# Optimization experiments

Measured on AMD Instinct MI355X. Metric: run time of the kernel, lower is better.

Reference implementation:

```python
import jax, jax.numpy as jnp
import numpy as np

EPSILON = 0.5
B, N0, N1, N_DIM = 128, 128, 128, 32


def setup_inputs() -> dict:
    key = jax.random.key(0)
    ks = jax.random.split(key, 7)
    X = jax.random.normal(ks[0], (B, N_DIM), dtype=jnp.float32)
    t = jax.random.uniform(ks[1], (1,), dtype=jnp.float32, minval=0.05, maxval=0.95)
    Mu0 = jax.random.normal(ks[2], (N0, N_DIM), dtype=jnp.float32)
    Mu1 = jax.random.normal(ks[3], (N1, N_DIM), dtype=jnp.float32)
    # positive diagonal variances
    S0 = jax.random.uniform(ks[4], (N0, N_DIM), dtype=jnp.float32) + 0.5
    S1 = jax.random.uniform(ks[5], (N1, N_DIM), dtype=jnp.float32) + 0.5
    # nonnegative coupling that sums to 1 (stand-in for the EMD plan)
    Lam = jax.random.uniform(ks[6], (N0, N1), dtype=jnp.float32)
    Lam = Lam / jnp.sum(Lam)
    return {"X": X, "t": t, "Mu0": Mu0, "Mu1": Mu1, "S0": S0, "S1": S1, "Lam": Lam}


def reference(X, t, Mu0, Mu1, S0, S1, Lam):
    """GMMflow.calc_u: Gaussian-mixture weighted drift u(X, t)."""
    eps = EPSILON
    t = t.reshape(())  # scalar time
    S0b = S0[:, None, :]   # [N0, 1, n]
    S1b = S1[None, :, :]   # [1, N1, n]
    Ds = jnp.sqrt(4.0 * S0b * S1b + eps ** 4)          # [N0, N1, n]
    Cs = 0.5 * (Ds - eps ** 2)
    Sigma = ((1 - t) ** 2) * S0b + (t ** 2) * S1b + 2 * t * (1 - t) * Cs + (eps ** 2) * t * (1 - t)
    Pt = t * S1b + (1 - t) * Cs
    Qt = (1 - t) * S0b + t * Cs
    St = Pt - Qt - (eps ** 2) * t
    Mut = (1 - t) * Mu0[:, None, :] + t * Mu1[None, :, :]   # [N0, N1, n]
    v = Mu1[None, :, :] - Mu0[:, None, :]                   # [N0, N1, n]
    K = St / Sigma                                          # [N0, N1, n]

    D = X[:, None, None, :] - Mut[None]                     # [B, N0, N1, n]
    U = K[None] * D + v[None]                               # [B, N0, N1, n]
    # Independent-Normal log_prob with the +n/2*log(2*pi) offset cancelled
    logw = jnp.sum(-0.5 * D * D / Sigma[None] - 0.5 * jnp.log(Sigma)[None], axis=-1)  # [B, N0, N1]
    W = jnp.exp(jnp.clip(logw, -50.0, 50.0)) * Lam[None]    # [B, N0, N1]

    num = jnp.einsum('bijn,bij->bn', U, W)                  # weighted drift sum
    den = jnp.sum(W, axis=(1, 2))                           # [B]
    return num / den[:, None]
```

## Files before the change

### kernel.cpp

```cpp
#include <hip/hip_runtime.h>
#include <math.h>

#define BB 128
#define ND 32
#define NIJ 16384
#define EPS2 0.25f
#define EPS4 0.0625f

#define TIJ 64
#define NBLK (NIJ / TIJ)
#define NTHR 512
#define ROWF 132

#define XS_OFF  8448
#define CC_OFF  13056
#define LAM_OFF 13120
#define LDS_FL  13184
#define STG_ROW 36

#define PART_STRIDE 4224
#define DEN_OFF_P 4096

__global__ __launch_bounds__(NTHR, 2) void gmm_fused(
    const float* __restrict__ Xg,
    const float* __restrict__ tptr,
    const float* __restrict__ Mu0, const float* __restrict__ Mu1,
    const float* __restrict__ S0,  const float* __restrict__ S1,
    const float* __restrict__ Lam,
    float* __restrict__ part)
{
    __shared__ __align__(16) float lds[LDS_FL];

    const int tid  = threadIdx.x;
    const int blk  = blockIdx.x;
    const int ij0g = blk * TIJ;
    const float t   = tptr[0];
    const float omt = 1.0f - t;

#pragma unroll
    for (int k = 0; k < (BB * ND) / NTHR; ++k) {
        const int idx = tid + k * NTHR;
        lds[XS_OFF + (idx >> 5) * STG_ROW + (idx & 31)] = Xg[idx];
    }

#pragma unroll
    for (int k = 0; k < (TIJ * ND) / NTHR; ++k) {
        const int idx = tid + k * NTHR;
        const int ijl = idx >> 5;
        const int n   = idx & 31;
        const int ij  = ij0g + ijl;
        const int i   = ij >> 7;
        const int j   = ij & 127;
        const float s0  = S0[i * ND + n];
        const float s1  = S1[j * ND + n];
        const float mu0 = Mu0[i * ND + n];
        const float mu1 = Mu1[j * ND + n];
        const float Ds  = sqrtf(4.0f * s0 * s1 + EPS4);
        const float Cs  = 0.5f * (Ds - EPS2);
        const float Sigma = omt * omt * s0 + t * t * s1
                          + 2.0f * t * omt * Cs + EPS2 * t * omt;
        const float St  = (t * s1 + omt * Cs) - (omt * s0 + t * Cs) - EPS2 * t;
        const float Mut = omt * mu0 + t * mu1;
        const float v   = mu1 - mu0;
        const float invS = 1.0f / Sigma;
        const float Kf  = St * invS;
        const float cA  = -0.5f * invS;
        const float cB  = Mut * invS;
        lds[ijl * ROWF + n]      = cA;
        lds[ijl * ROWF + 32 + n] = cB;
        lds[ijl * ROWF + 64 + n] = Kf;
        lds[ijl * ROWF + 96 + n] = v - Kf * Mut;
        float cc = cA * Mut * Mut - 0.5f * __logf(Sigma);
        cc += __shfl_xor(cc, 1);
        cc += __shfl_xor(cc, 2);
        cc += __shfl_xor(cc, 4);
        cc += __shfl_xor(cc, 8);
        cc += __shfl_xor(cc, 16);
        if (n == 0) lds[CC_OFF + ijl] = cc;
    }
    if (tid < TIJ) lds[LAM_OFF + tid] = Lam[ij0g + tid];

    __syncthreads();

    const int gij = tid & 7;
    const int bl  = tid >> 3;

    float x0[ND], x1[ND];
#pragma unroll
    for (int c = 0; c < 8; ++c) {
        const float4 v4 = *(const float4*)&lds[XS_OFF + bl * STG_ROW + 4 * c];
        const float4 w4 = *(const float4*)&lds[XS_OFF + (bl + 64) * STG_ROW + 4 * c];
        x0[4*c+0] = v4.x; x0[4*c+1] = v4.y; x0[4*c+2] = v4.z; x0[4*c+3] = v4.w;
        x1[4*c+0] = w4.x; x1[4*c+1] = w4.y; x1[4*c+2] = w4.z; x1[4*c+3] = w4.w;
    }

    float num0[ND], num1[ND];
#pragma unroll
    for (int n = 0; n < ND; ++n) { num0[n] = 0.0f; num1[n] = 0.0f; }
    float den0 = 0.0f, den1 = 0.0f;

#pragma unroll
    for (int it = 0; it < TIJ / 8; ++it) {
        const int ijl = gij + (it << 3);
        const float* __restrict__ row = &lds[ijl * ROWF];
        const float cc0 = lds[CC_OFF + ijl];
        float la0 = cc0, lb0 = 0.0f;
        float la1 = cc0, lb1 = 0.0f;
#pragma unroll
        for (int nc = 0; nc < 8; ++nc) {
            const float4 a  = *(const float4*)&row[nc * 4];
            const float4 bq = *(const float4*)&row[32 + nc * 4];
            la0 = fmaf(fmaf(a.x, x0[nc*4+0], bq.x), x0[nc*4+0], la0);
            lb0 = fmaf(fmaf(a.y, x0[nc*4+1], bq.y), x0[nc*4+1], lb0);
            la0 = fmaf(fmaf(a.z, x0[nc*4+2], bq.z), x0[nc*4+2], la0);
            lb0 = fmaf(fmaf(a.w, x0[nc*4+3], bq.w), x0[nc*4+3], lb0);
            la1 = fmaf(fmaf(a.x, x1[nc*4+0], bq.x), x1[nc*4+0], la1);
            lb1 = fmaf(fmaf(a.y, x1[nc*4+1], bq.y), x1[nc*4+1], lb1);
            la1 = fmaf(fmaf(a.z, x1[nc*4+2], bq.z), x1[nc*4+2], la1);
            lb1 = fmaf(fmaf(a.w, x1[nc*4+3], bq.w), x1[nc*4+3], lb1);
        }
        float lw0 = fminf(fmaxf(la0 + lb0, -50.0f), 50.0f);
        float lw1 = fminf(fmaxf(la1 + lb1, -50.0f), 50.0f);
        const float lam = lds[LAM_OFF + ijl];
        const float w0 = __expf(lw0) * lam;
        const float w1 = __expf(lw1) * lam;
        den0 += w0; den1 += w1;
#pragma unroll
        for (int nc = 0; nc < 8; ++nc) {
            const float4 kk = *(const float4*)&row[64 + nc * 4];
            const float4 kv = *(const float4*)&row[96 + nc * 4];
            num0[nc*4+0] = fmaf(w0, fmaf(kk.x, x0[nc*4+0], kv.x), num0[nc*4+0]);
            num0[nc*4+1] = fmaf(w0, fmaf(kk.y, x0[nc*4+1], kv.y), num0[nc*4+1]);
            num0[nc*4+2] = fmaf(w0, fmaf(kk.z, x0[nc*4+2], kv.z), num0[nc*4+2]);
            num0[nc*4+3] = fmaf(w0, fmaf(kk.w, x0[nc*4+3], kv.w), num0[nc*4+3]);
            num1[nc*4+0] = fmaf(w1, fmaf(kk.x, x1[nc*4+0], kv.x), num1[nc*4+0]);
            num1[nc*4+1] = fmaf(w1, fmaf(kk.y, x1[nc*4+1], kv.y), num1[nc*4+1]);
            num1[nc*4+2] = fmaf(w1, fmaf(kk.z, x1[nc*4+2], kv.z), num1[nc*4+2]);
            num1[nc*4+3] = fmaf(w1, fmaf(kk.w, x1[nc*4+3], kv.w), num1[nc*4+3]);
        }
    }

#pragma unroll
    for (int c = 0; c < 16; ++c) {
        const float s0v = (gij & 4) ? num0[c] : num0[c + 16];
        const float s1v = (gij & 4) ? num1[c] : num1[c + 16];
        const float r0 = __shfl_xor(s0v, 4);
        const float r1 = __shfl_xor(s1v, 4);
        num0[c] = ((gij & 4) ? num0[c + 16] : num0[c]) + r0;
        num1[c] = ((gij & 4) ? num1[c + 16] : num1[c]) + r1;
    }
#pragma unroll
    for (int c = 0; c < 8; ++c) {
        const float s0v = (gij & 2) ? num0[c] : num0[c + 8];
        const float s1v = (gij & 2) ? num1[c] : num1[c + 8];
        const float r0 = __shfl_xor(s0v, 2);
        const float r1 = __shfl_xor(s1v, 2);
        num0[c] = ((gij & 2) ? num0[c + 8] : num0[c]) + r0;
        num1[c] = ((gij & 2) ? num1[c + 8] : num1[c]) + r1;
    }
#pragma unroll
    for (int c = 0; c < 4; ++c) {
        const float s0v = (gij & 1) ? num0[c] : num0[c + 4];
        const float s1v = (gij & 1) ? num1[c] : num1[c + 4];
        const float r0 = __shfl_xor(s0v, 1);
        const float r1 = __shfl_xor(s1v, 1);
        num0[c] = ((gij & 1) ? num0[c + 4] : num0[c]) + r0;
        num1[c] = ((gij & 1) ? num1[c + 4] : num1[c]) + r1;
    }

    den0 += __shfl_xor(den0, 1);
    den0 += __shfl_xor(den0, 2);
    den0 += __shfl_xor(den0, 4);
    den1 += __shfl_xor(den1, 1);
    den1 += __shfl_xor(den1, 2);
    den1 += __shfl_xor(den1, 4);

    float* __restrict__ dstg = part + (size_t)blk * PART_STRIDE;
    *(float4*)(dstg + bl * 32 + gij * 4) =
        make_float4(num0[0], num0[1], num0[2], num0[3]);
    *(float4*)(dstg + (bl + 64) * 32 + gij * 4) =
        make_float4(num1[0], num1[1], num1[2], num1[3]);
    if (gij == 0) {
        dstg[DEN_OFF_P + bl]      = den0;
        dstg[DEN_OFF_P + bl + 64] = den1;
    }
}

__global__ __launch_bounds__(256) void gmm_reduce(
    const float* __restrict__ part,
    float* __restrict__ out)
{
    const int blk = blockIdx.x;
    const int b   = blk >> 1;
    const int nh  = blk & 1;
    const int tid = threadIdx.x;
    const int n16 = tid & 15;
    const int sg  = tid >> 4;
    const int n   = nh * 16 + n16;

    float num = 0.0f, den = 0.0f;
#pragma unroll
    for (int g = 0; g < 16; ++g) {
        const int s = sg + g * 16;
        const size_t base = (size_t)s * PART_STRIDE;
        num += part[base + b * 32 + n];
        den += part[base + DEN_OFF_P + b];
    }

    __shared__ float red[16][18];
    red[sg][n16] = num;
    if (n16 == 0) red[sg][16] = den;
    __syncthreads();

    if (tid < 16) {
        float ns = 0.0f, ds = 0.0f;
#pragma unroll
        for (int k = 0; k < 16; ++k) {
            ns += red[k][tid];
            ds += red[k][16];
        }
        out[b * 32 + nh * 16 + tid] = ns / ds;
    }
}

extern "C" void kernel_launch(void* const* d_in, const int* in_sizes, int n_in,
                              void* d_out, int out_size, void* d_ws, size_t ws_size,
                              hipStream_t stream)
{
    const float* X   = (const float*)d_in[0];
    const float* t   = (const float*)d_in[1];
    const float* Mu0 = (const float*)d_in[2];
    const float* Mu1 = (const float*)d_in[3];
    const float* S0  = (const float*)d_in[4];
    const float* S1  = (const float*)d_in[5];
    const float* Lam = (const float*)d_in[6];
    float* out  = (float*)d_out;
    float* part = (float*)d_ws;

    gmm_fused<<<NBLK, NTHR, 0, stream>>>(X, t, Mu0, Mu1, S0, S1, Lam, part);
    gmm_reduce<<<2 * BB, 256, 0, stream>>>(part, out);
}
```

Baseline: 88.84 us.

## Split feature dimension across thread pairs and double block size to 1024 threads

Each thread now handles 16 of the 32 feature dimensions instead of all 32, with a cross-lane shuffle combining the partial log-weights. The block grows to 1024 threads, which halves the per-thread register arrays and should let more waves be resident to hide LDS latency. The cost is an extra shuffle per weight, exp computed redundantly by both halves, and smaller writes in the final reduction. X staging also becomes a single float4 load per thread.

```diff
diff --git a/kernel.cpp b/kernel.cpp
--- a/kernel.cpp
+++ b/kernel.cpp
@@ -9,7 +9,7 @@
 
 #define TIJ 64
 #define NBLK (NIJ / TIJ)
-#define NTHR 512
+#define NTHR 1024
 #define ROWF 132
 
 #define XS_OFF  8448
@@ -21,7 +21,7 @@
 #define PART_STRIDE 4224
 #define DEN_OFF_P 4096
 
-__global__ __launch_bounds__(NTHR, 2) void gmm_fused(
+__global__ __launch_bounds__(NTHR, 4) void gmm_fused(
     const float* __restrict__ Xg,
     const float* __restrict__ tptr,
     const float* __restrict__ Mu0, const float* __restrict__ Mu1,
@@ -37,10 +37,11 @@
     const float t   = tptr[0];
     const float omt = 1.0f - t;
 
-#pragma unroll
-    for (int k = 0; k < (BB * ND) / NTHR; ++k) {
-        const int idx = tid + k * NTHR;
-        lds[XS_OFF + (idx >> 5) * STG_ROW + (idx & 31)] = Xg[idx];
+    {
+        const int r  = tid >> 3;
+        const int c4 = (tid & 7) * 4;
+        *(float4*)&lds[XS_OFF + r * STG_ROW + c4] =
+            *(const float4*)&Xg[tid * 4];
     }
 
 #pragma unroll
@@ -83,31 +84,32 @@
     __syncthreads();
 
     const int gij = tid & 7;
-    const int bl  = tid >> 3;
-
-    float x0[ND], x1[ND];
-#pragma unroll
-    for (int c = 0; c < 8; ++c) {
-        const float4 v4 = *(const float4*)&lds[XS_OFF + bl * STG_ROW + 4 * c];
-        const float4 w4 = *(const float4*)&lds[XS_OFF + (bl + 64) * STG_ROW + 4 * c];
+    const int nh  = (tid >> 3) & 1;
+    const int bl  = tid >> 4;
+    const int n0  = nh * 16;
+
+    float x0[16], x1[16];
+#pragma unroll
+    for (int c = 0; c < 4; ++c) {
+        const float4 v4 = *(const float4*)&lds[XS_OFF + bl * STG_ROW + n0 + 4 * c];
+        const float4 w4 = *(const float4*)&lds[XS_OFF + (bl + 64) * STG_ROW + n0 + 4 * c];
         x0[4*c+0] = v4.x; x0[4*c+1] = v4.y; x0[4*c+2] = v4.z; x0[4*c+3] = v4.w;
         x1[4*c+0] = w4.x; x1[4*c+1] = w4.y; x1[4*c+2] = w4.z; x1[4*c+3] = w4.w;
     }
 
-    float num0[ND], num1[ND];
-#pragma unroll
-    for (int n = 0; n < ND; ++n) { num0[n] = 0.0f; num1[n] = 0.0f; }
+    float num0[16], num1[16];
+#pragma unroll
+    for (int n = 0; n < 16; ++n) { num0[n] = 0.0f; num1[n] = 0.0f; }
     float den0 = 0.0f, den1 = 0.0f;
 
-#pragma unroll
+#pragma unroll 2
     for (int it = 0; it < TIJ / 8; ++it) {
         const int ijl = gij + (it << 3);
-        const float* __restrict__ row = &lds[ijl * ROWF];
-        const float cc0 = lds[CC_OFF + ijl];
-        float la0 = cc0, lb0 = 0.0f;
-        float la1 = cc0, lb1 = 0.0f;
-#pragma unroll
-        for (int nc = 0; nc < 8; ++nc) {
+        const float* __restrict__ row = &lds[ijl * ROWF + n0];
+        float la0 = 0.0f, lb0 = 0.0f;
+        float la1 = 0.0f, lb1 = 0.0f;
+#pragma unroll
+        for (int nc = 0; nc < 4; ++nc) {
             const float4 a  = *(const float4*)&row[nc * 4];
             const float4 bq = *(const float4*)&row[32 + nc * 4];
             la0 = fmaf(fmaf(a.x, x0[nc*4+0], bq.x), x0[nc*4+0], la0);
@@ -119,14 +121,17 @@
             la1 = fmaf(fmaf(a.z, x1[nc*4+2], bq.z), x1[nc*4+2], la1);
             lb1 = fmaf(fmaf(a.w, x1[nc*4+3], bq.w), x1[nc*4+3], lb1);
         }
-        float lw0 = fminf(fmaxf(la0 + lb0, -50.0f), 50.0f);
-        float lw1 = fminf(fmaxf(la1 + lb1, -50.0f), 50.0f);
+        float lw0 = la0 + lb0;  lw0 += __shfl_xor(lw0, 8);
+        float lw1 = la1 + lb1;  lw1 += __shfl_xor(lw1, 8);
+        const float cc0 = lds[CC_OFF + ijl];
         const float lam = lds[LAM_OFF + ijl];
+        lw0 = fminf(fmaxf(lw0 + cc0, -50.0f), 50.0f);
+        lw1 = fminf(fmaxf(lw1 + cc0, -50.0f), 50.0f);
         const float w0 = __expf(lw0) * lam;
         const float w1 = __expf(lw1) * lam;
         den0 += w0; den1 += w1;
 #pragma unroll
-        for (int nc = 0; nc < 8; ++nc) {
+        for (int nc = 0; nc < 4; ++nc) {
             const float4 kk = *(const float4*)&row[64 + nc * 4];
             const float4 kv = *(const float4*)&row[96 + nc * 4];
             num0[nc*4+0] = fmaf(w0, fmaf(kk.x, x0[nc*4+0], kv.x), num0[nc*4+0]);
@@ -141,31 +146,31 @@
     }
 
 #pragma unroll
-    for (int c = 0; c < 16; ++c) {
-        const float s0v = (gij & 4) ? num0[c] : num0[c + 16];
-        const float s1v = (gij & 4) ? num1[c] : num1[c + 16];
+    for (int c = 0; c < 8; ++c) {
+        const float s0v = (gij & 4) ? num0[c] : num0[c + 8];
+        const float s1v = (gij & 4) ? num1[c] : num1[c + 8];
         const float r0 = __shfl_xor(s0v, 4);
         const float r1 = __shfl_xor(s1v, 4);
-        num0[c] = ((gij & 4) ? num0[c + 16] : num0[c]) + r0;
-        num1[c] = ((gij & 4) ? num1[c + 16] : num1[c]) + r1;
-    }
-#pragma unroll
-    for (int c = 0; c < 8; ++c) {
-        const float s0v = (gij & 2) ? num0[c] : num0[c + 8];
-        const float s1v = (gij & 2) ? num1[c] : num1[c + 8];
+        num0[c] = ((gij & 4) ? num0[c + 8] : num0[c]) + r0;
+        num1[c] = ((gij & 4) ? num1[c + 8] : num1[c]) + r1;
+    }
+#pragma unroll
+    for (int c = 0; c < 4; ++c) {
+        const float s0v = (gij & 2) ? num0[c] : num0[c + 4];
+        const float s1v = (gij & 2) ? num1[c] : num1[c + 4];
         const float r0 = __shfl_xor(s0v, 2);
         const float r1 = __shfl_xor(s1v, 2);
-        num0[c] = ((gij & 2) ? num0[c + 8] : num0[c]) + r0;
-        num1[c] = ((gij & 2) ? num1[c + 8] : num1[c]) + r1;
-    }
-#pragma unroll
-    for (int c = 0; c < 4; ++c) {
-        const float s0v = (gij & 1) ? num0[c] : num0[c + 4];
-        const float s1v = (gij & 1) ? num1[c] : num1[c + 4];
+        num0[c] = ((gij & 2) ? num0[c + 4] : num0[c]) + r0;
+        num1[c] = ((gij & 2) ? num1[c + 4] : num1[c]) + r1;
+    }
+#pragma unroll
+    for (int c = 0; c < 2; ++c) {
+        const float s0v = (gij & 1) ? num0[c] : num0[c + 2];
+        const float s1v = (gij & 1) ? num1[c] : num1[c + 2];
         const float r0 = __shfl_xor(s0v, 1);
         const float r1 = __shfl_xor(s1v, 1);
-        num0[c] = ((gij & 1) ? num0[c + 4] : num0[c]) + r0;
-        num1[c] = ((gij & 1) ? num1[c + 4] : num1[c]) + r1;
+        num0[c] = ((gij & 1) ? num0[c + 2] : num0[c]) + r0;
+        num1[c] = ((gij & 1) ? num1[c + 2] : num1[c]) + r1;
     }
 
     den0 += __shfl_xor(den0, 1);
@@ -176,11 +181,11 @@
     den1 += __shfl_xor(den1, 4);
 
     float* __restrict__ dstg = part + (size_t)blk * PART_STRIDE;
-    *(float4*)(dstg + bl * 32 + gij * 4) =
-        make_float4(num0[0], num0[1], num0[2], num0[3]);
-    *(float4*)(dstg + (bl + 64) * 32 + gij * 4) =
-        make_float4(num1[0], num1[1], num1[2], num1[3]);
-    if (gij == 0) {
+    *(float2*)(dstg + bl * 32 + n0 + 2 * gij) =
+        make_float2(num0[0], num0[1]);
+    *(float2*)(dstg + (bl + 64) * 32 + n0 + 2 * gij) =
+        make_float2(num1[0], num1[1]);
+    if ((tid & 15) == 0) {
         dstg[DEN_OFF_P + bl]      = den0;
         dstg[DEN_OFF_P + bl + 64] = den1;
     }
```

Result: faster. 81.37 us (-8.4%).
